# Kernel tuning notes

Measured on AMD Instinct MI355X. Metric: run time of the kernel, lower is better.

Reference implementation:

```python
import jax, jax.numpy as jnp
import numpy as np

B, N, V, H = 8, 2048, 256, 1024
EPS = 1e-5
NEG = -1e9


def _layernorm(x, g, b):
    m = jnp.mean(x, axis=-1, keepdims=True)
    v = jnp.mean((x - m) ** 2, axis=-1, keepdims=True)
    return (x - m) / jnp.sqrt(v + EPS) * g + b


def setup_inputs() -> dict:
    key = jax.random.key(0)
    ks = jax.random.split(key, 10)
    tril = jnp.tril(jnp.ones((N, N), jnp.float32))
    return {
        "h": jax.random.normal(ks[0], (B, N, V), jnp.float32),
        "mask_one": tril,                      # keep causal entries
        "mask_zero": NEG * (1.0 - tril),       # -inf-ish above diagonal
        "ln_attn_g": jnp.ones((V,), jnp.float32),
        "ln_attn_b": jnp.zeros((V,), jnp.float32),
        "ln_mlp_g": jnp.ones((V,), jnp.float32),
        "ln_mlp_b": jnp.zeros((V,), jnp.float32),
        "wv": jax.random.normal(ks[1], (V,), jnp.float32),
        "wv_bos": jax.random.normal(ks[2], (V,), jnp.float32),
        "wo_w": jax.random.normal(ks[3], (V, V), jnp.float32) / np.sqrt(V),
        "qk_bos": jax.random.normal(ks[4], (V,), jnp.float32),
        "qk_previous": jax.random.normal(ks[5], (V,), jnp.float32),
        "qk_direction": jnp.ones((V,), jnp.float32),  # middel_layer=False, frozen
        "w1": jax.random.normal(ks[6], (H, V), jnp.float32) / np.sqrt(V),
        "w2": jax.random.normal(ks[7], (V, H), jnp.float32) / np.sqrt(H),
    }


def reference(h, mask_one, mask_zero, ln_attn_g, ln_attn_b, ln_mlp_g, ln_mlp_b,
              wv, wv_bos, wo_w, qk_bos, qk_previous, qk_direction, w1, w2):
    b, n, v = h.shape
    # mask blends LayerNorm only into row 0 (BOS position)
    attn_input = h.at[:, 0, :].set(_layernorm(h[:, 0, :], ln_attn_g, ln_attn_b))
    # value states: diag(wv) on positions 1.., wo(wv_bos) at position 0
    values = attn_input[:, 1:, :] * wv                      # [B, N-1, V]
    v_bos = wo_w @ wv_bos                                   # Linear(bias=False)
    values = jnp.concatenate(
        [jnp.broadcast_to(v_bos, (b, 1, v)), values], axis=1)  # [B, N, V]
    # sparse QK logits: column 0 term + sub-diagonal term, densified then masked
    col0 = (attn_input @ qk_bos) * (attn_input[:, 0, :] @ qk_direction)[:, None]  # [B, N]
    d = attn_input @ qk_previous                            # [B, N]
    qk = jnp.zeros((b, n, n), h.dtype).at[:, :, 0].add(col0)
    idx = jnp.arange(1, n)
    qk = qk.at[:, idx, idx - 1].add(d[:, 1:])               # row r, col r-1 = d[:, r]
    qk = qk * mask_one + mask_zero
    attn_out = jax.nn.softmax(qk, axis=-1) @ values         # [B, N, V]
    # FFN branch with its own BOS-only LayerNorm blend
    mlp_input = h.at[:, 0, :].set(_layernorm(h[:, 0, :], ln_mlp_g, ln_mlp_b))
    mlp_out = jax.nn.relu(mlp_input @ w1.T) @ w2.T          # [B, N, V]
    return attn_out + mlp_out
```

## Files before the change

kernel.cpp:

```cpp
#include <hip/hip_runtime.h>
#include <hip/hip_bf16.h>

#define BB 8
#define NN 2048
#define VV 256
#define HH 1024
#define CHK 64
#define RPC 32
constexpr float EPS = 1e-5f;

typedef __attribute__((ext_vector_type(4))) float floatx4;
typedef __attribute__((ext_vector_type(8))) short short8;

__device__ __forceinline__ void load_lds16(const void* g, void* l) {
    __builtin_amdgcn_global_load_lds((const __attribute__((address_space(1))) void*)g,
                                     (__attribute__((address_space(3))) void*)l, 16, 0, 0);
}
__device__ __forceinline__ float bf16s_to_f(short s) {
    unsigned u = ((unsigned)(unsigned short)s) << 16;
    return __builtin_bit_cast(float, u);
}

__global__ void prep_kernel(const float* __restrict__ h,
                            const float* __restrict__ g_attn, const float* __restrict__ b_attn,
                            const float* __restrict__ g_mlp,  const float* __restrict__ b_mlp,
                            const float* __restrict__ qk_dir,
                            const float* __restrict__ wo_w,  const float* __restrict__ wv_bos,
                            float* __restrict__ attn_row0, float* __restrict__ mlp_row0,
                            float* __restrict__ v_bos, float* __restrict__ sum0)
{
    int t = threadIdx.x;
    __shared__ float red[VV];
    if (blockIdx.x < BB) {
        int b = blockIdx.x;
        float x = h[(size_t)b * NN * VV + t];
        red[t] = x; __syncthreads();
        for (int s = 128; s > 0; s >>= 1) { if (t < s) red[t] += red[t + s]; __syncthreads(); }
        float m = red[0] * (1.0f / VV); __syncthreads();
        float xc = x - m;
        red[t] = xc * xc; __syncthreads();
        for (int s = 128; s > 0; s >>= 1) { if (t < s) red[t] += red[t + s]; __syncthreads(); }
        float var = red[0] * (1.0f / VV); __syncthreads();
        float inv = 1.0f / sqrtf(var + EPS);
        float an = xc * inv * g_attn[t] + b_attn[t];
        float mn = xc * inv * g_mlp[t] + b_mlp[t];
        attn_row0[b * VV + t] = an;
        mlp_row0[b * VV + t]  = mn;
        red[t] = an * qk_dir[t]; __syncthreads();
        for (int s = 128; s > 0; s >>= 1) { if (t < s) red[t] += red[t + s]; __syncthreads(); }
        if (t == 0) sum0[b] = red[0];
    } else {
        const float4* wp = reinterpret_cast<const float4*>(wo_w + (size_t)t * VV);
        const float4* vp = reinterpret_cast<const float4*>(wv_bos);
        float acc = 0.f;
        for (int j = 0; j < VV / 4; ++j) {
            float4 a = wp[j], b = vp[j];
            acc += a.x * b.x + a.y * b.y + a.z * b.z + a.w * b.w;
        }
        v_bos[t] = acc;
    }
}

__global__ __launch_bounds__(256) void scan_qkw_cvt_kernel(
    const float* __restrict__ h, const float* __restrict__ mlp_row0,
    const float* __restrict__ wv,
    const float* __restrict__ qk_bos, const float* __restrict__ qk_prev,
    const float* __restrict__ sum0,
    short* __restrict__ Xb,
    float* __restrict__ wpack,
    float* __restrict__ chunkSum,
    const float* __restrict__ w1, const float* __restrict__ w2,
    short* __restrict__ w1b, short* __restrict__ w2b)
{
    __shared__ float lds[4][VV];
    int wave = threadIdx.x >> 6, lane = threadIdx.x & 63;
    int b = blockIdx.x / CHK, c = blockIdx.x % CHK;
    int r0 = c * RPC + wave * 8;
    float4 wv4 = reinterpret_cast<const float4*>(wv)[lane];
    float4 qb4 = reinterpret_cast<const float4*>(qk_bos)[lane];
    float4 qp4 = reinterpret_cast<const float4*>(qk_prev)[lane];
    float s0b = sum0[b];
    float4 vsum = {0.f, 0.f, 0.f, 0.f};
#pragma unroll
    for (int rr = 0; rr < 8; ++rr) {
        int r = r0 + rr;
        size_t base = ((size_t)b * NN + r) * VV;
        float4 x = *reinterpret_cast<const float4*>(h + base + lane * 4);
        float4 xs = x;
        if (r == 0) xs = *reinterpret_cast<const float4*>(mlp_row0 + b * VV + lane * 4);
        __hip_bfloat16 c0 = __float2bfloat16(xs.x), c1 = __float2bfloat16(xs.y),
                       c2 = __float2bfloat16(xs.z), c3 = __float2bfloat16(xs.w);
        short4 pk;
        pk.x = *reinterpret_cast<short*>(&c0);
        pk.y = *reinterpret_cast<short*>(&c1);
        pk.z = *reinterpret_cast<short*>(&c2);
        pk.w = *reinterpret_cast<short*>(&c3);
        *reinterpret_cast<short4*>(Xb + base + lane * 4) = pk;
        if (r != 0) {
            vsum.x += bf16s_to_f(pk.x) * wv4.x; vsum.y += bf16s_to_f(pk.y) * wv4.y;
            vsum.z += bf16s_to_f(pk.z) * wv4.z; vsum.w += bf16s_to_f(pk.w) * wv4.w;
        }
        float s1 = x.x * qb4.x + x.y * qb4.y + x.z * qb4.z + x.w * qb4.w;
        float s2 = x.x * qp4.x + x.y * qp4.y + x.z * qp4.z + x.w * qp4.w;
        for (int off = 32; off > 0; off >>= 1) {
            s1 += __shfl_down(s1, off);
            s2 += __shfl_down(s2, off);
        }
        if (lane == 0) {
            int gid = b * NN + r;
            float W0, WP, WZ;
            if (r == 0) { W0 = 1.f; WP = 0.f; WZ = 0.f; }
            else if (r == 1) {
                float a = s1 * s0b + s2;
                float m = fmaxf(a, 0.f);
                float ea = expf(a - m), ez = expf(-m);
                float Z = ea + ez;
                W0 = ea / Z; WZ = ez / Z; WP = WZ;
            } else {
                float a = s1 * s0b;
                float m = fmaxf(fmaxf(a, s2), 0.f);
                float ea = expf(a - m), ed = expf(s2 - m), ez = expf(-m);
                float Z = ea + ed + (float)(r - 1) * ez;
                W0 = ea / Z; WP = ed / Z; WZ = ez / Z;
            }
            float4 wp4 = {W0, WP - WZ, WZ, 0.f};
            *reinterpret_cast<float4*>(wpack + (size_t)gid * 4) = wp4;
        }
    }
    reinterpret_cast<float4*>(lds[wave])[lane] = vsum;

    {
        int gi = blockIdx.x * 256 + threadIdx.x;
        size_t off = (size_t)gi * 4;
        const float* src; short* dst;
        if (off < (size_t)HH * VV) { src = w1 + off; dst = w1b + off; }
        else                       { src = w2 + (off - (size_t)HH * VV); dst = w2b + (off - (size_t)HH * VV); }
        float4 x = *reinterpret_cast<const float4*>(src);
        __hip_bfloat16 c0 = __float2bfloat16(x.x), c1 = __float2bfloat16(x.y),
                       c2 = __float2bfloat16(x.z), c3 = __float2bfloat16(x.w);
        short4 pk;
        pk.x = *reinterpret_cast<short*>(&c0);
        pk.y = *reinterpret_cast<short*>(&c1);
        pk.z = *reinterpret_cast<short*>(&c2);
        pk.w = *reinterpret_cast<short*>(&c3);
        *reinterpret_cast<short4*>(dst) = pk;
    }

    __syncthreads();
    int v = threadIdx.x;
    chunkSum[((size_t)b * CHK + c) * VV + v] = lds[0][v] + lds[1][v] + lds[2][v] + lds[3][v];
}

__global__ void chunkscan_kernel(float* __restrict__ chunkSum)
{
    int b = blockIdx.x, v = threadIdx.x;
    float vals[CHK];
#pragma unroll
    for (int c = 0; c < CHK; ++c) vals[c] = chunkSum[(b * CHK + c) * VV + v];
    float run = 0.f;
#pragma unroll
    for (int c = 0; c < CHK; ++c) { float t = vals[c]; vals[c] = run; run += t; }
#pragma unroll
    for (int c = 0; c < CHK; ++c) chunkSum[(b * CHK + c) * VV + v] = vals[c];
}

__global__ __launch_bounds__(512) void mlp_fused4(const short* __restrict__ Xb,
                                                  const short* __restrict__ w1b,
                                                  const short* __restrict__ w2b,
                                                  const float* __restrict__ wv,
                                                  const float* __restrict__ v_bos,
                                                  const float* __restrict__ wpack,
                                                  const float* __restrict__ chunkSum,
                                                  float* __restrict__ out)
{
    __shared__ __align__(16) char smem[136 * 1024];
    short (*sW1)[64 * 256] = reinterpret_cast<short(*)[64 * 256]>(smem);
    short (*sW2)[256 * 64] = reinterpret_cast<short(*)[256 * 64]>(smem + 65536);
    short* sY = reinterpret_cast<short*>(smem + 131072);

    int wave = threadIdx.x >> 6, lane = threadIdx.x & 63;
    int wm = wave >> 2, wn = wave & 3;
    int ra = lane & 15, q = lane >> 4;
    int m0 = blockIdx.x * 64;

    short8 xf[8][2];
#pragma unroll
    for (int ks = 0; ks < 8; ++ks)
#pragma unroll
        for (int i = 0; i < 2; ++i)
            xf[ks][i] = *reinterpret_cast<const short8*>(
                Xb + (size_t)(m0 + wm * 32 + i * 16 + ra) * VV + ks * 32 + q * 8);

    floatx4 oacc[2][4];
#pragma unroll
    for (int i = 0; i < 2; ++i)
#pragma unroll
        for (int j = 0; j < 4; ++j) oacc[i][j] = floatx4{0.f, 0.f, 0.f, 0.f};

    auto stage = [&](int hc, int buf) {
#pragma unroll
        for (int it = 0; it < 4; ++it) {
            int g = wave * 4 + it;
            int n = g * 2 + (lane >> 5);
            int slot = lane & 31;
            load_lds16(w1b + (size_t)(hc * 64 + n) * VV + (slot ^ (n & 7)) * 8,
                       &sW1[buf][g * 512]);
        }
#pragma unroll
        for (int it = 0; it < 4; ++it) {
            int g = wave * 4 + it;
            int v = g * 8 + (lane >> 3);
            int slot = lane & 7;
            load_lds16(w2b + (size_t)v * HH + hc * 64 + (slot ^ (v & 7)) * 8,
                       &sW2[buf][g * 512]);
        }
    };

    stage(0, 0);
    for (int hc = 0; hc < 16; ++hc) {
        int p = hc & 1;
        __syncthreads();
        if (hc < 15) stage(hc + 1, p ^ 1);

        floatx4 yacc[2];
        yacc[0] = floatx4{0.f, 0.f, 0.f, 0.f};
        yacc[1] = floatx4{0.f, 0.f, 0.f, 0.f};
        int nb = wn * 16 + ra;
#pragma unroll
        for (int ks = 0; ks < 8; ++ks) {
            short8 bfr = *reinterpret_cast<const short8*>(
                &sW1[p][nb * 256 + (((ks * 4 + q) ^ (ra & 7)) * 8)]);
#pragma unroll
            for (int i = 0; i < 2; ++i)
                yacc[i] = __builtin_amdgcn_mfma_f32_16x16x32_bf16(xf[ks][i], bfr, yacc[i], 0, 0, 0);
        }
#pragma unroll
        for (int i = 0; i < 2; ++i)
#pragma unroll
            for (int reg = 0; reg < 4; ++reg) {
                int m = wm * 32 + i * 16 + q * 4 + reg;
                int ke = wn * 16 + ra;
                __hip_bfloat16 hb = __float2bfloat16(fmaxf(yacc[i][reg], 0.f));
                sY[m * 64 + (((ke >> 3) ^ (m & 7)) * 8) + (ke & 7)] =
                    *reinterpret_cast<short*>(&hb);
            }
        __syncthreads();

#pragma unroll
        for (int kk = 0; kk < 2; ++kk) {
            short8 a2[2];
#pragma unroll
            for (int i = 0; i < 2; ++i) {
                int m = wm * 32 + i * 16 + ra;
                a2[i] = *reinterpret_cast<const short8*>(
                    &sY[m * 64 + (((kk * 4 + q) ^ (ra & 7)) * 8)]);
            }
#pragma unroll
            for (int j = 0; j < 4; ++j) {
                int v = wn * 64 + j * 16 + ra;
                short8 b2 = *reinterpret_cast<const short8*>(
                    &sW2[p][v * 64 + (((kk * 4 + q) ^ (ra & 7)) * 8)]);
#pragma unroll
                for (int i = 0; i < 2; ++i)
                    oacc[i][j] = __builtin_amdgcn_mfma_f32_16x16x32_bf16(a2[i], b2, oacc[i][j], 0, 0, 0);
            }
        }
    }

    __syncthreads();
    float* sOut = reinterpret_cast<float*>(smem);
#pragma unroll
    for (int i = 0; i < 2; ++i)
#pragma unroll
        for (int j = 0; j < 4; ++j)
#pragma unroll
            for (int reg = 0; reg < 4; ++reg) {
                int l = wm * 32 + i * 16 + q * 4 + reg;
                int col = wn * 64 + j * 16 + ra;
                sOut[l * 260 + col] = oacc[i][j][reg];
            }
    __syncthreads();

    {
        int v    = threadIdx.x & 255;
        int half = threadIdx.x >> 8;
        int b  = m0 >> 11;
        int n0 = m0 & (NN - 1);
        int r0 = n0 + half * RPC;
        float wvv = wv[v];
        float vb  = v_bos[v];
        float S = chunkSum[((size_t)b * CHK + (r0 >> 5)) * VV + v];
        float prev = 0.f;
        int r = r0;
        if (r0 == 0) {
            out[((size_t)b * NN) * VV + v] = vb + sOut[0 * 260 + v];
            r = 1;
        } else {
            short p = Xb[((size_t)b * NN + r0 - 1) * VV + v];
            prev = bf16s_to_f(p) * wvv;
        }
#pragma unroll 4
        for (; r < r0 + RPC; ++r) {
            size_t idx = ((size_t)b * NN + r) * VV + v;
            float val = bf16s_to_f(Xb[idx]) * wvv;
            S += val;
            float4 wp4 = *reinterpret_cast<const float4*>(wpack + (size_t)(b * NN + r) * 4);
            float o = wp4.x * vb + wp4.y * prev + wp4.z * S;
            prev = val;
            out[idx] = o + sOut[(r - n0) * 260 + v];
        }
    }
}

extern "C" void kernel_launch(void* const* d_in, const int* in_sizes, int n_in,
                              void* d_out, int out_size, void* d_ws, size_t ws_size,
                              hipStream_t stream)
{
    const float* h        = (const float*)d_in[0];
    const float* ln_attn_g = (const float*)d_in[3];
    const float* ln_attn_b = (const float*)d_in[4];
    const float* ln_mlp_g  = (const float*)d_in[5];
    const float* ln_mlp_b  = (const float*)d_in[6];
    const float* wv        = (const float*)d_in[7];
    const float* wv_bos    = (const float*)d_in[8];
    const float* wo_w      = (const float*)d_in[9];
    const float* qk_bos    = (const float*)d_in[10];
    const float* qk_prev   = (const float*)d_in[11];
    const float* qk_dir    = (const float*)d_in[12];
    const float* w1        = (const float*)d_in[13];
    const float* w2        = (const float*)d_in[14];
    float* out = (float*)d_out;

    float* attn_row0 = (float*)d_ws;
    float* mlp_row0  = attn_row0 + BB * VV;
    float* v_bos     = mlp_row0 + BB * VV;
    float* sum0      = v_bos + VV;
    float* wpack     = sum0 + 8;
    float* chunkSum  = wpack + (size_t)BB * NN * 4;
    short* Xb        = (short*)(chunkSum + BB * CHK * VV);
    short* w1b       = (short*)(Xb + (size_t)BB * NN * VV);
    short* w2b       = w1b + HH * VV;

    prep_kernel<<<BB + 1, 256, 0, stream>>>(h, ln_attn_g, ln_attn_b, ln_mlp_g, ln_mlp_b,
                                            qk_dir, wo_w, wv_bos,
                                            attn_row0, mlp_row0, v_bos, sum0);
    scan_qkw_cvt_kernel<<<BB * CHK, 256, 0, stream>>>(h, mlp_row0, wv, qk_bos, qk_prev,
                                                      sum0, Xb, wpack, chunkSum,
                                                      w1, w2, w1b, w2b);
    chunkscan_kernel<<<BB, 256, 0, stream>>>(chunkSum);
    mlp_fused4<<<256, 512, 0, stream>>>(Xb, w1b, w2b, wv, v_bos, wpack, chunkSum, out);
}
```

Measured before the change: 163.1 us.

## Fold prep and chunk-scan kernels into neighbours, cutting launches from four to two

Each scan block now recomputes the BOS-row LayerNorm and qk_direction dot product redundantly using wave shuffles, and block 0 computes v_bos, which removes the separate prep kernel. The chunk prefix-scan kernel is also removed: each MLP block sums the preceding chunk sums directly, overlapped with the first weight staging. This trades two kernel launches and their dependency gaps for redundant per-block work, namely up to 63 strided loads per thread in the MLP epilogue prefix and a LayerNorm per scan block.

```diff
diff --git a/kernel.cpp b/kernel.cpp
--- a/kernel.cpp
+++ b/kernel.cpp
@@ -21,65 +21,54 @@
     return __builtin_bit_cast(float, u);
 }
 
-__global__ void prep_kernel(const float* __restrict__ h,
-                            const float* __restrict__ g_attn, const float* __restrict__ b_attn,
-                            const float* __restrict__ g_mlp,  const float* __restrict__ b_mlp,
-                            const float* __restrict__ qk_dir,
-                            const float* __restrict__ wo_w,  const float* __restrict__ wv_bos,
-                            float* __restrict__ attn_row0, float* __restrict__ mlp_row0,
-                            float* __restrict__ v_bos, float* __restrict__ sum0)
-{
-    int t = threadIdx.x;
-    __shared__ float red[VV];
-    if (blockIdx.x < BB) {
-        int b = blockIdx.x;
-        float x = h[(size_t)b * NN * VV + t];
-        red[t] = x; __syncthreads();
-        for (int s = 128; s > 0; s >>= 1) { if (t < s) red[t] += red[t + s]; __syncthreads(); }
-        float m = red[0] * (1.0f / VV); __syncthreads();
-        float xc = x - m;
-        red[t] = xc * xc; __syncthreads();
-        for (int s = 128; s > 0; s >>= 1) { if (t < s) red[t] += red[t + s]; __syncthreads(); }
-        float var = red[0] * (1.0f / VV); __syncthreads();
-        float inv = 1.0f / sqrtf(var + EPS);
-        float an = xc * inv * g_attn[t] + b_attn[t];
-        float mn = xc * inv * g_mlp[t] + b_mlp[t];
-        attn_row0[b * VV + t] = an;
-        mlp_row0[b * VV + t]  = mn;
-        red[t] = an * qk_dir[t]; __syncthreads();
-        for (int s = 128; s > 0; s >>= 1) { if (t < s) red[t] += red[t + s]; __syncthreads(); }
-        if (t == 0) sum0[b] = red[0];
-    } else {
-        const float4* wp = reinterpret_cast<const float4*>(wo_w + (size_t)t * VV);
-        const float4* vp = reinterpret_cast<const float4*>(wv_bos);
-        float acc = 0.f;
-        for (int j = 0; j < VV / 4; ++j) {
-            float4 a = wp[j], b = vp[j];
-            acc += a.x * b.x + a.y * b.y + a.z * b.z + a.w * b.w;
-        }
-        v_bos[t] = acc;
-    }
-}
-
-__global__ __launch_bounds__(256) void scan_qkw_cvt_kernel(
-    const float* __restrict__ h, const float* __restrict__ mlp_row0,
+__global__ __launch_bounds__(256) void scan_fused_kernel(
+    const float* __restrict__ h,
+    const float* __restrict__ g_attn, const float* __restrict__ b_attn,
+    const float* __restrict__ g_mlp,  const float* __restrict__ b_mlp,
+    const float* __restrict__ qk_dir,
+    const float* __restrict__ wo_w,  const float* __restrict__ wv_bos,
     const float* __restrict__ wv,
     const float* __restrict__ qk_bos, const float* __restrict__ qk_prev,
-    const float* __restrict__ sum0,
     short* __restrict__ Xb,
     float* __restrict__ wpack,
     float* __restrict__ chunkSum,
+    float* __restrict__ v_bos,
     const float* __restrict__ w1, const float* __restrict__ w2,
     short* __restrict__ w1b, short* __restrict__ w2b)
 {
     __shared__ float lds[4][VV];
-    int wave = threadIdx.x >> 6, lane = threadIdx.x & 63;
+    __shared__ __align__(16) float mrow[VV];
+    __shared__ float redA[4], redB[4], redC[4];
+    int t = threadIdx.x;
+    int wave = t >> 6, lane = t & 63;
     int b = blockIdx.x / CHK, c = blockIdx.x % CHK;
+
+    float x0 = h[(size_t)b * NN * VV + t];
+    float s = x0;
+    for (int off = 32; off > 0; off >>= 1) s += __shfl_down(s, off);
+    if (lane == 0) redA[wave] = s;
+    __syncthreads();
+    float m = (redA[0] + redA[1] + redA[2] + redA[3]) * (1.0f / VV);
+    float xc = x0 - m;
+    float sv = xc * xc;
+    for (int off = 32; off > 0; off >>= 1) sv += __shfl_down(sv, off);
+    if (lane == 0) redB[wave] = sv;
+    __syncthreads();
+    float var = (redB[0] + redB[1] + redB[2] + redB[3]) * (1.0f / VV);
+    float inv = 1.0f / sqrtf(var + EPS);
+    float an = xc * inv * g_attn[t] + b_attn[t];
+    float mn = xc * inv * g_mlp[t]  + b_mlp[t];
+    float sd = an * qk_dir[t];
+    for (int off = 32; off > 0; off >>= 1) sd += __shfl_down(sd, off);
+    if (lane == 0) redC[wave] = sd;
+    mrow[t] = mn;
+    __syncthreads();
+    float s0b = redC[0] + redC[1] + redC[2] + redC[3];
+
     int r0 = c * RPC + wave * 8;
     float4 wv4 = reinterpret_cast<const float4*>(wv)[lane];
     float4 qb4 = reinterpret_cast<const float4*>(qk_bos)[lane];
     float4 qp4 = reinterpret_cast<const float4*>(qk_prev)[lane];
-    float s0b = sum0[b];
     float4 vsum = {0.f, 0.f, 0.f, 0.f};
 #pragma unroll
     for (int rr = 0; rr < 8; ++rr) {
@@ -87,7 +76,7 @@
         size_t base = ((size_t)b * NN + r) * VV;
         float4 x = *reinterpret_cast<const float4*>(h + base + lane * 4);
         float4 xs = x;
-        if (r == 0) xs = *reinterpret_cast<const float4*>(mlp_row0 + b * VV + lane * 4);
+        if (r == 0) xs = *reinterpret_cast<const float4*>(&mrow[lane * 4]);
         __hip_bfloat16 c0 = __float2bfloat16(xs.x), c1 = __float2bfloat16(xs.y),
                        c2 = __float2bfloat16(xs.z), c3 = __float2bfloat16(xs.w);
         short4 pk;
@@ -112,14 +101,14 @@
             if (r == 0) { W0 = 1.f; WP = 0.f; WZ = 0.f; }
             else if (r == 1) {
                 float a = s1 * s0b + s2;
-                float m = fmaxf(a, 0.f);
-                float ea = expf(a - m), ez = expf(-m);
+                float mm = fmaxf(a, 0.f);
+                float ea = expf(a - mm), ez = expf(-mm);
                 float Z = ea + ez;
                 W0 = ea / Z; WZ = ez / Z; WP = WZ;
             } else {
                 float a = s1 * s0b;
-                float m = fmaxf(fmaxf(a, s2), 0.f);
-                float ea = expf(a - m), ed = expf(s2 - m), ez = expf(-m);
+                float mm = fmaxf(fmaxf(a, s2), 0.f);
+                float ea = expf(a - mm), ed = expf(s2 - mm), ez = expf(-mm);
                 float Z = ea + ed + (float)(r - 1) * ez;
                 W0 = ea / Z; WP = ed / Z; WZ = ez / Z;
             }
@@ -146,25 +135,23 @@
         *reinterpret_cast<short4*>(dst) = pk;
     }
 
+    if (blockIdx.x == 0) {
+        const float4* wp = reinterpret_cast<const float4*>(wo_w + (size_t)t * VV);
+        const float4* vp = reinterpret_cast<const float4*>(wv_bos);
+        float acc = 0.f;
+        for (int j = 0; j < VV / 4; ++j) {
+            float4 a = wp[j], bq = vp[j];
+            acc += a.x * bq.x + a.y * bq.y + a.z * bq.z + a.w * bq.w;
+        }
+        v_bos[t] = acc;
+    }
+
     __syncthreads();
     int v = threadIdx.x;
     chunkSum[((size_t)b * CHK + c) * VV + v] = lds[0][v] + lds[1][v] + lds[2][v] + lds[3][v];
 }
 
-__global__ void chunkscan_kernel(float* __restrict__ chunkSum)
-{
-    int b = blockIdx.x, v = threadIdx.x;
-    float vals[CHK];
-#pragma unroll
-    for (int c = 0; c < CHK; ++c) vals[c] = chunkSum[(b * CHK + c) * VV + v];
-    float run = 0.f;
-#pragma unroll
-    for (int c = 0; c < CHK; ++c) { float t = vals[c]; vals[c] = run; run += t; }
-#pragma unroll
-    for (int c = 0; c < CHK; ++c) chunkSum[(b * CHK + c) * VV + v] = vals[c];
-}
-
-__global__ __launch_bounds__(512) void mlp_fused4(const short* __restrict__ Xb,
+__global__ __launch_bounds__(512) void mlp_fused5(const short* __restrict__ Xb,
                                                   const short* __restrict__ w1b,
                                                   const short* __restrict__ w2b,
                                                   const float* __restrict__ wv,
@@ -182,20 +169,8 @@
     int wm = wave >> 2, wn = wave & 3;
     int ra = lane & 15, q = lane >> 4;
     int m0 = blockIdx.x * 64;
-
-    short8 xf[8][2];
-#pragma unroll
-    for (int ks = 0; ks < 8; ++ks)
-#pragma unroll
-        for (int i = 0; i < 2; ++i)
-            xf[ks][i] = *reinterpret_cast<const short8*>(
-                Xb + (size_t)(m0 + wm * 32 + i * 16 + ra) * VV + ks * 32 + q * 8);
-
-    floatx4 oacc[2][4];
-#pragma unroll
-    for (int i = 0; i < 2; ++i)
-#pragma unroll
-        for (int j = 0; j < 4; ++j) oacc[i][j] = floatx4{0.f, 0.f, 0.f, 0.f};
+    int bq = m0 >> 11;
+    int n0 = m0 & (NN - 1);
 
     auto stage = [&](int hc, int buf) {
 #pragma unroll
@@ -217,6 +192,31 @@
     };
 
     stage(0, 0);
+
+    short8 xf[8][2];
+#pragma unroll
+    for (int ks = 0; ks < 8; ++ks)
+#pragma unroll
+        for (int i = 0; i < 2; ++i)
+            xf[ks][i] = *reinterpret_cast<const short8*>(
+                Xb + (size_t)(m0 + wm * 32 + i * 16 + ra) * VV + ks * 32 + q * 8);
+
+    int vcol = threadIdx.x & 255;
+    int half = threadIdx.x >> 8;
+    int cpre = (n0 >> 5) + half;
+    float Sreg = 0.f;
+    {
+        const float* cs = chunkSum + (size_t)(bq * CHK) * VV + vcol;
+#pragma unroll 4
+        for (int c2 = 0; c2 < cpre; ++c2) Sreg += cs[(size_t)c2 * VV];
+    }
+
+    floatx4 oacc[2][4];
+#pragma unroll
+    for (int i = 0; i < 2; ++i)
+#pragma unroll
+        for (int j = 0; j < 4; ++j) oacc[i][j] = floatx4{0.f, 0.f, 0.f, 0.f};
+
     for (int hc = 0; hc < 16; ++hc) {
         int p = hc & 1;
         __syncthreads();
@@ -238,10 +238,10 @@
         for (int i = 0; i < 2; ++i)
 #pragma unroll
             for (int reg = 0; reg < 4; ++reg) {
-                int m = wm * 32 + i * 16 + q * 4 + reg;
+                int mrow_ = wm * 32 + i * 16 + q * 4 + reg;
                 int ke = wn * 16 + ra;
                 __hip_bfloat16 hb = __float2bfloat16(fmaxf(yacc[i][reg], 0.f));
-                sY[m * 64 + (((ke >> 3) ^ (m & 7)) * 8) + (ke & 7)] =
+                sY[mrow_ * 64 + (((ke >> 3) ^ (mrow_ & 7)) * 8) + (ke & 7)] =
                     *reinterpret_cast<short*>(&hb);
             }
         __syncthreads();
@@ -251,9 +251,9 @@
             short8 a2[2];
 #pragma unroll
             for (int i = 0; i < 2; ++i) {
-                int m = wm * 32 + i * 16 + ra;
+                int mrow_ = wm * 32 + i * 16 + ra;
                 a2[i] = *reinterpret_cast<const short8*>(
-                    &sY[m * 64 + (((kk * 4 + q) ^ (ra & 7)) * 8)]);
+                    &sY[mrow_ * 64 + (((kk * 4 + q) ^ (ra & 7)) * 8)]);
             }
 #pragma unroll
             for (int j = 0; j < 4; ++j) {
@@ -282,32 +282,28 @@
     __syncthreads();
 
     {
-        int v    = threadIdx.x & 255;
-        int half = threadIdx.x >> 8;
-        int b  = m0 >> 11;
-        int n0 = m0 & (NN - 1);
         int r0 = n0 + half * RPC;
-        float wvv = wv[v];
-        float vb  = v_bos[v];
-        float S = chunkSum[((size_t)b * CHK + (r0 >> 5)) * VV + v];
+        float wvv = wv[vcol];
+        float vb  = v_bos[vcol];
+        float S = Sreg;
         float prev = 0.f;
         int r = r0;
         if (r0 == 0) {
-            out[((size_t)b * NN) * VV + v] = vb + sOut[0 * 260 + v];
+            out[((size_t)bq * NN) * VV + vcol] = vb + sOut[0 * 260 + vcol];
             r = 1;
         } else {
-            short p = Xb[((size_t)b * NN + r0 - 1) * VV + v];
+            short p = Xb[((size_t)bq * NN + r0 - 1) * VV + vcol];
             prev = bf16s_to_f(p) * wvv;
         }
 #pragma unroll 4
         for (; r < r0 + RPC; ++r) {
-            size_t idx = ((size_t)b * NN + r) * VV + v;
+            size_t idx = ((size_t)bq * NN + r) * VV + vcol;
             float val = bf16s_to_f(Xb[idx]) * wvv;
             S += val;
-            float4 wp4 = *reinterpret_cast<const float4*>(wpack + (size_t)(b * NN + r) * 4);
+            float4 wp4 = *reinterpret_cast<const float4*>(wpack + (size_t)(bq * NN + r) * 4);
             float o = wp4.x * vb + wp4.y * prev + wp4.z * S;
             prev = val;
-            out[idx] = o + sOut[(r - n0) * 260 + v];
+            out[idx] = o + sOut[(r - n0) * 260 + vcol];
         }
     }
 }
@@ -331,22 +327,17 @@
     const float* w2        = (const float*)d_in[14];
     float* out = (float*)d_out;
 
-    float* attn_row0 = (float*)d_ws;
-    float* mlp_row0  = attn_row0 + BB * VV;
-    float* v_bos     = mlp_row0 + BB * VV;
-    float* sum0      = v_bos + VV;
-    float* wpack     = sum0 + 8;
+    float* v_bos     = (float*)d_ws;
+    float* wpack     = v_bos + VV;
     float* chunkSum  = wpack + (size_t)BB * NN * 4;
     short* Xb        = (short*)(chunkSum + BB * CHK * VV);
     short* w1b       = (short*)(Xb + (size_t)BB * NN * VV);
     short* w2b       = w1b + HH * VV;
 
-    prep_kernel<<<BB + 1, 256, 0, stream>>>(h, ln_attn_g, ln_attn_b, ln_mlp_g, ln_mlp_b,
-                                            qk_dir, wo_w, wv_bos,
-                                            attn_row0, mlp_row0, v_bos, sum0);
-    scan_qkw_cvt_kernel<<<BB * CHK, 256, 0, stream>>>(h, mlp_row0, wv, qk_bos, qk_prev,
-                                                      sum0, Xb, wpack, chunkSum,
-                                                      w1, w2, w1b, w2b);
-    chunkscan_kernel<<<BB, 256, 0, stream>>>(chunkSum);
-    mlp_fused4<<<256, 512, 0, stream>>>(Xb, w1b, w2b, wv, v_bos, wpack, chunkSum, out);
-}
+    scan_fused_kernel<<<BB * CHK, 256, 0, stream>>>(h, ln_attn_g, ln_attn_b,
+                                                    ln_mlp_g, ln_mlp_b, qk_dir,
+                                                    wo_w, wv_bos, wv, qk_bos, qk_prev,
+                                                    Xb, wpack, chunkSum, v_bos,
+                                                    w1, w2, w1b, w2b);
+    mlp_fused5<<<256, 512, 0, stream>>>(Xb, w1b, w2b, wv, v_bos, wpack, chunkSum, out);
+}
```

Measured after the change: 154.4 us. -5.4%, faster.
